# Kernel tuning notes

Measured on AMD Instinct MI355X. Metric: run time of the kernel, lower is better.

The kernel has to match this reference:

```python
import jax, jax.numpy as jnp
import numpy as np

B, S, D = 2, 2048, 2048
H, DK, DV, L = 16, 128, 128, 64


def setup_inputs() -> dict:
    key = jax.random.key(0)
    ks = jax.random.split(key, 16)
    sc = lambda fan_in: 1.0 / np.sqrt(fan_in)
    inp = {
        "queries": jax.random.normal(ks[0], (B, S, D), jnp.float32),
        "keys": jax.random.normal(ks[1], (B, S, D), jnp.float32),
        "values": jax.random.normal(ks[2], (B, S, D), jnp.float32),
        # weights stored [in, out]
        "Wq": jax.random.normal(ks[3], (D, DK * H), jnp.float32) * sc(D),
        "bq": jnp.zeros((DK * H,), jnp.float32),
        "Wlk": jax.random.normal(ks[4], (D, L * H), jnp.float32) * sc(D),
        "blk": jnp.zeros((L * H,), jnp.float32),
        "Wlv": jax.random.normal(ks[5], (D, L * H), jnp.float32) * sc(D),
        "blv": jnp.zeros((L * H,), jnp.float32),
        "Wkr": jax.random.normal(ks[6], (L, DK), jnp.float32) * sc(L),
        "bkr": jnp.zeros((DK,), jnp.float32),
        "Wvr": jax.random.normal(ks[7], (L, DV), jnp.float32) * sc(L),
        "bvr": jnp.zeros((DV,), jnp.float32),
        "Wo": jax.random.normal(ks[8], (DV * H, D), jnp.float32) * sc(DV * H),
        "bo": jnp.zeros((D,), jnp.float32),
    }
    return inp


def reference(queries, keys, values, Wq, bq, Wlk, blk, Wlv, blv, Wkr, bkr, Wvr, bvr, Wo, bo):
    b, sq, _ = queries.shape
    sk = keys.shape[1]
    # query projection -> [b, h, sq, dk]
    q = (queries @ Wq + bq).reshape(b, sq, H, DK).transpose(0, 2, 1, 3)
    # low-rank latent KV -> [b, sk, h, L]
    lat_k = (keys @ Wlk + blk).reshape(b, sk, H, L)
    lat_v = (values @ Wlv + blv).reshape(b, sk, H, L)
    # reconstruction -> [b, h, sk, dk/dv]
    k = (lat_k @ Wkr + bkr).transpose(0, 2, 1, 3)
    v = (lat_v @ Wvr + bvr).transpose(0, 2, 1, 3)
    scores = jnp.einsum("bhqd,bhkd->bhqk", q, k) / np.sqrt(DK).astype(np.float32)
    causal = jnp.triu(jnp.ones((sq, sk), dtype=bool), k=1)
    scores = jnp.where(causal, -jnp.inf, scores)
    attn = jax.nn.softmax(scores, axis=-1)
    out = jnp.einsum("bhqk,bhkd->bhqd", attn, v)
    out = out.transpose(0, 2, 1, 3).reshape(b, sq, H * DV)
    return out @ Wo + bo
```

## Files before the change

kernel.cpp:

```cpp
#include <hip/hip_runtime.h>
#include <hip/hip_bf16.h>

#define B_SZ    2
#define S_LEN   2048
#define D_MODEL 2048
#define N_HEADS 16
#define D_HEAD  128
#define L_RANK  64
#define M_ROWS  (B_SZ * S_LEN)
#define KD      2048
#define NT      (KD / 32)
#define NTK     (KD / 64)

typedef short          bf16x8 __attribute__((ext_vector_type(8)));
typedef float          f32x4  __attribute__((ext_vector_type(4)));
typedef float          f32x16 __attribute__((ext_vector_type(16)));
typedef unsigned short us4v   __attribute__((ext_vector_type(4)));
typedef unsigned short us8v   __attribute__((ext_vector_type(8)));
typedef unsigned int   u32x4  __attribute__((ext_vector_type(4)));

#define SCALE_Q 0.127517432f

static __device__ __forceinline__ unsigned short f2bf(float f) {
    unsigned int u = __float_as_uint(f);
    u += 0x7FFFu + ((u >> 16) & 1u);
    return (unsigned short)(u >> 16);
}

static __device__ __forceinline__ void gload16(const void* g, void* l) {
    __builtin_amdgcn_global_load_lds(
        (const __attribute__((address_space(1))) unsigned int*)g,
        (__attribute__((address_space(3))) unsigned int*)l, 16, 0, 0);
}

static __device__ __forceinline__ bf16x8 ds_read128(const unsigned short* p) {
    bf16x8 r;
    unsigned int a = (unsigned int)(size_t)
        (const __attribute__((address_space(3))) unsigned short*)p;
    asm volatile("ds_read_b128 %0, %1" : "=&v"(r) : "v"(a));
    return r;
}

static __device__ __forceinline__ float exp2_hw(float x) {
    float r; asm("v_exp_f32 %0, %1" : "=v"(r) : "v"(x)); return r;
}
static __device__ __forceinline__ unsigned int cvtpk_bf16(float a, float b) {
    unsigned int r; asm("v_cvt_pk_bf16_f32 %0, %1, %2" : "=v"(r) : "v"(a), "v"(b)); return r;
}

__global__ __launch_bounds__(256) void prep_kernel(
    const float* __restrict__ q_in, const float* __restrict__ k_in,
    const float* __restrict__ v_in,
    const float* __restrict__ Wq, const float* __restrict__ Wlk,
    const float* __restrict__ Wlv, const float* __restrict__ Wo,
    const float* __restrict__ Wkr, const float* __restrict__ Wvr,
    unsigned short* __restrict__ q_o, unsigned short* __restrict__ k_o,
    unsigned short* __restrict__ v_o,
    unsigned short* __restrict__ WqT, unsigned short* __restrict__ WlkT,
    unsigned short* __restrict__ WlvT, unsigned short* __restrict__ WoT,
    unsigned short* __restrict__ WkrT, unsigned short* __restrict__ WvrT)
{
    __shared__ float tl[64][69];
    const int bid = blockIdx.x, tid = threadIdx.x;

    if (bid < 12288) {
        const int z = bid >> 12;
        const float* in = z == 0 ? q_in : (z == 1 ? k_in : v_in);
        unsigned short* out = z == 0 ? q_o : (z == 1 ? k_o : v_o);
        size_t i = ((size_t)(bid & 4095) * 256 + tid) * 8;
        float4 a = *(const float4*)&in[i];
        float4 b = *(const float4*)&in[i + 4];
        us8v o = { f2bf(a.x), f2bf(a.y), f2bf(a.z), f2bf(a.w),
                   f2bf(b.x), f2bf(b.y), f2bf(b.z), f2bf(b.w) };
        *(us8v*)&out[i] = o;
    } else if (bid < 16384) {
        const int t = bid - 12288;
        const int z = t >> 10;
        const int y = (t & 1023) >> 5, x = t & 31;
        const int Nz = (z == 1 || z == 2) ? 1024 : 2048;
        if (x * 64 >= Nz) return;
        const float* W = z == 0 ? Wq : (z == 1 ? Wlk : (z == 2 ? Wlv : Wo));
        unsigned short* WT = z == 0 ? WqT : (z == 1 ? WlkT : (z == 2 ? WlvT : WoT));
        const int k0 = y * 64, n0 = x * 64;
        #pragma unroll
        for (int c = 0; c < 4; ++c) {
            int idx = c * 256 + tid;
            int r = idx >> 4, c4 = (idx & 15) * 4;
            float4 v = *(const float4*)&W[(size_t)(k0 + r) * Nz + n0 + c4];
            tl[r][c4] = v.x; tl[r][c4 + 1] = v.y; tl[r][c4 + 2] = v.z; tl[r][c4 + 3] = v.w;
        }
        __syncthreads();
        #pragma unroll
        for (int c = 0; c < 2; ++c) {
            int idx = c * 256 + tid;
            int nr = idx >> 3, s = idx & 7;
            us8v o;
            #pragma unroll
            for (int j = 0; j < 8; ++j) o[j] = f2bf(tl[s * 8 + j][nr]);
            *(us8v*)&WT[(size_t)(n0 + nr) * KD + k0 + s * 8] = o;
        }
    } else {
        #pragma unroll 1
        for (int t2 = 0; t2 < 2; ++t2) {
            const float* W = t2 ? Wvr : Wkr;
            unsigned short* WT = t2 ? WvrT : WkrT;
            for (int i = 0; i < 32; ++i) {
                int e = i * 256 + tid;
                int d = e >> 6, l = e & 63;
                WT[d * 64 + l] = f2bf(W[l * 128 + d]);
            }
        }
    }
}

__global__ __launch_bounds__(512) void stage1_8p_kernel(
    const unsigned short* __restrict__ Aq, const unsigned short* __restrict__ Ak,
    const unsigned short* __restrict__ Av,
    const unsigned short* __restrict__ WqT, const unsigned short* __restrict__ WlkT,
    const unsigned short* __restrict__ WlvT,
    const float* __restrict__ bq, const float* __restrict__ blk,
    const float* __restrict__ blv,
    unsigned short* __restrict__ q_bf, unsigned short* __restrict__ lat_k,
    unsigned short* __restrict__ lat_v)
{
    __shared__ unsigned short Al[2][2][256 * 32];
    __shared__ unsigned short Bl[2][2][256 * 32];

    const int bid = blockIdx.x;
    const int swz = (bid & 7) * 32 + (bid >> 3);
    int z, rem, row0, col0, Nz;
    if (swz < 128)      { z = 0; rem = swz;       row0 = (rem >> 3) * 256; col0 = (rem & 7) * 256; Nz = 2048; }
    else if (swz < 192) { z = 1; rem = swz - 128; row0 = (rem >> 2) * 256; col0 = (rem & 3) * 256; Nz = 1024; }
    else                { z = 2; rem = swz - 192; row0 = (rem >> 2) * 256; col0 = (rem & 3) * 256; Nz = 1024; }

    const unsigned short* A    = z == 0 ? Aq  : (z == 1 ? Ak   : Av);
    const unsigned short* Bt   = z == 0 ? WqT : (z == 1 ? WlkT : WlvT);
    const float*          bias = z == 0 ? bq  : (z == 1 ? blk  : blv);
    unsigned short*       C    = z == 0 ? q_bf : (z == 1 ? lat_k : lat_v);

    const int tid = threadIdx.x;
    const int lane = tid & 63, wid = tid >> 6;
    const int lr = lane & 15, lg = lane >> 4;
    const int wm = wid >> 2, wn = wid & 3;

    const int lin0 = tid, lin1 = 512 + tid;
    const int rS0 = lin0 >> 2, rS1 = lin1 >> 2;
    const int cS0 = (lin0 & 3) ^ ((rS0 >> 1) & 3);
    const int cS1 = (lin1 & 3) ^ ((rS1 >> 1) & 3);
    const unsigned short* aS0 = A  + (size_t)(row0 + rS0) * KD + cS0 * 8;
    const unsigned short* aS1 = A  + (size_t)(row0 + rS1) * KD + cS1 * 8;
    const unsigned short* bS0 = Bt + (size_t)(col0 + rS0) * KD + cS0 * 8;
    const unsigned short* bS1 = Bt + (size_t)(col0 + rS1) * KD + cS1 * 8;
    const int d0 = lin0 * 8, d1 = lin1 * 8;

    int aoff[8], boff[4];
    #pragma unroll
    for (int m = 0; m < 8; ++m) {
        int row = wm * 128 + m * 16 + lr;
        aoff[m] = row * 32 + ((lg ^ ((row >> 1) & 3)) * 8);
    }
    #pragma unroll
    for (int n = 0; n < 4; ++n) {
        int row = wn * 64 + n * 16 + lr;
        boff[n] = row * 32 + ((lg ^ ((row >> 1) & 3)) * 8);
    }

    f32x4 acc[8][4];
    #pragma unroll
    for (int m = 0; m < 8; ++m)
        #pragma unroll
        for (int n = 0; n < 4; ++n) acc[m][n] = (f32x4){0.f, 0.f, 0.f, 0.f};

#define STAGE_A(buf, kh, kt) do { \
        gload16(aS0 + (size_t)(kt) * 64 + (kh) * 32, &Al[buf][kh][d0]); \
        gload16(aS1 + (size_t)(kt) * 64 + (kh) * 32, &Al[buf][kh][d1]); } while (0)
#define STAGE_B(buf, kh, kt) do { \
        gload16(bS0 + (size_t)(kt) * 64 + (kh) * 32, &Bl[buf][kh][d0]); \
        gload16(bS1 + (size_t)(kt) * 64 + (kh) * 32, &Bl[buf][kh][d1]); } while (0)

    STAGE_A(0, 0, 0); STAGE_B(0, 0, 0); STAGE_A(0, 1, 0); STAGE_B(0, 1, 0);

    #pragma unroll 1
    for (int t = 0; t < NTK; ++t) {
        const int cur = t & 1, nxt = cur ^ 1;
        const bool more = (t + 1 < NTK);

        asm volatile("s_waitcnt vmcnt(4)" ::: "memory");
        __builtin_amdgcn_s_barrier();
        asm volatile("" ::: "memory");

        bf16x8 af[8], bf0, bf1;
        if (more) STAGE_A(nxt, 0, t + 1);
        #pragma unroll
        for (int m = 0; m < 8; ++m) af[m] = ds_read128(&Al[cur][0][aoff[m]]);
        bf0 = ds_read128(&Bl[cur][0][boff[0]]);
        bf1 = ds_read128(&Bl[cur][0][boff[1]]);
        asm volatile("s_waitcnt lgkmcnt(0)" ::: "memory");
        __builtin_amdgcn_sched_barrier(0);
        __builtin_amdgcn_s_setprio(1);
        #pragma unroll
        for (int m = 0; m < 8; ++m) {
            acc[m][0] = __builtin_amdgcn_mfma_f32_16x16x32_bf16(af[m], bf0, acc[m][0], 0, 0, 0);
            acc[m][1] = __builtin_amdgcn_mfma_f32_16x16x32_bf16(af[m], bf1, acc[m][1], 0, 0, 0);
        }
        __builtin_amdgcn_s_setprio(0);

        if (more) STAGE_B(nxt, 0, t + 1);
        bf0 = ds_read128(&Bl[cur][0][boff[2]]);
        bf1 = ds_read128(&Bl[cur][0][boff[3]]);
        asm volatile("s_waitcnt lgkmcnt(0)" ::: "memory");
        __builtin_amdgcn_sched_barrier(0);
        __builtin_amdgcn_s_setprio(1);
        #pragma unroll
        for (int m = 0; m < 8; ++m) {
            acc[m][2] = __builtin_amdgcn_mfma_f32_16x16x32_bf16(af[m], bf0, acc[m][2], 0, 0, 0);
            acc[m][3] = __builtin_amdgcn_mfma_f32_16x16x32_bf16(af[m], bf1, acc[m][3], 0, 0, 0);
        }
        __builtin_amdgcn_s_setprio(0);

        if (more) asm volatile("s_waitcnt vmcnt(4)" ::: "memory");
        else      asm volatile("s_waitcnt vmcnt(0)" ::: "memory");
        __builtin_amdgcn_s_barrier();
        asm volatile("" ::: "memory");

        if (more) STAGE_A(nxt, 1, t + 1);
        #pragma unroll
        for (int m = 0; m < 8; ++m) af[m] = ds_read128(&Al[cur][1][aoff[m]]);
        bf0 = ds_read128(&Bl[cur][1][boff[0]]);
        bf1 = ds_read128(&Bl[cur][1][boff[1]]);
        asm volatile("s_waitcnt lgkmcnt(0)" ::: "memory");
        __builtin_amdgcn_sched_barrier(0);
        __builtin_amdgcn_s_setprio(1);
        #pragma unroll
        for (int m = 0; m < 8; ++m) {
            acc[m][0] = __builtin_amdgcn_mfma_f32_16x16x32_bf16(af[m], bf0, acc[m][0], 0, 0, 0);
            acc[m][1] = __builtin_amdgcn_mfma_f32_16x16x32_bf16(af[m], bf1, acc[m][1], 0, 0, 0);
        }
        __builtin_amdgcn_s_setprio(0);

        if (more) STAGE_B(nxt, 1, t + 1);
        bf0 = ds_read128(&Bl[cur][1][boff[2]]);
        bf1 = ds_read128(&Bl[cur][1][boff[3]]);
        asm volatile("s_waitcnt lgkmcnt(0)" ::: "memory");
        __builtin_amdgcn_sched_barrier(0);
        __builtin_amdgcn_s_setprio(1);
        #pragma unroll
        for (int m = 0; m < 8; ++m) {
            acc[m][2] = __builtin_amdgcn_mfma_f32_16x16x32_bf16(af[m], bf0, acc[m][2], 0, 0, 0);
            acc[m][3] = __builtin_amdgcn_mfma_f32_16x16x32_bf16(af[m], bf1, acc[m][3], 0, 0, 0);
        }
        __builtin_amdgcn_s_setprio(0);
    }
#undef STAGE_A
#undef STAGE_B

    float bv[4];
    #pragma unroll
    for (int n = 0; n < 4; ++n) bv[n] = bias[col0 + wn * 64 + n * 16 + lr];
    const float omul = (z == 0) ? SCALE_Q : 1.0f;

    #pragma unroll
    for (int m = 0; m < 8; ++m) {
        #pragma unroll
        for (int n = 0; n < 4; ++n) {
            const int col = col0 + wn * 64 + n * 16 + lr;
            const int rowb = row0 + wm * 128 + m * 16 + lg * 4;
            #pragma unroll
            for (int j = 0; j < 4; ++j)
                C[(size_t)(rowb + j) * Nz + col] = f2bf((acc[m][n][j] + bv[n]) * omul);
        }
    }
}

__global__ __launch_bounds__(256) void recon_kernel(
    const unsigned short* __restrict__ lat_k, const unsigned short* __restrict__ lat_v,
    const unsigned short* __restrict__ WkrT, const unsigned short* __restrict__ WvrT,
    const float* __restrict__ bkr, const float* __restrict__ bvr,
    unsigned short* __restrict__ k_bf, unsigned short* __restrict__ v_t)
{
    __shared__ unsigned short Alds[128 * 64];
    __shared__ unsigned short Blds[128 * 64];

    const int flat = blockIdx.x;
    const int swz = (flat & 7) * 128 + (flat >> 3);
    const int z = swz >> 9;
    const int rem = swz & 511;
    const int h = rem >> 5;
    const int r0 = (rem & 31) * 128;

    const unsigned short* lat = z ? lat_v : lat_k;
    const unsigned short* WT  = z ? WvrT : WkrT;
    const float* bias = z ? bvr : bkr;

    const int tid = threadIdx.x;
    const int lane = tid & 63, wid = tid >> 6;
    const int lr = lane & 15, lg = lane >> 4;
    const int wm = wid >> 1, wn = wid & 1;

    #pragma unroll
    for (int c = 0; c < 4; ++c) {
        int e = c * 256 + tid;
        int row = e >> 3, pc = e & 7;
        gload16(lat + (size_t)(r0 + row) * 1024 + h * 64 + ((pc ^ (row & 7)) * 8),
                Alds + e * 8);
    }
    #pragma unroll
    for (int c = 0; c < 4; ++c) {
        int e = c * 256 + tid;
        int d = e >> 3, pc = e & 7;
        gload16(WT + (size_t)d * 64 + ((pc ^ (d & 7)) * 8), Blds + e * 8);
    }
    __syncthreads();

    f32x4 acc[4][4];
    #pragma unroll
    for (int m = 0; m < 4; ++m)
        #pragma unroll
        for (int n = 0; n < 4; ++n) acc[m][n] = (f32x4){0.f, 0.f, 0.f, 0.f};

    #pragma unroll
    for (int ks = 0; ks < 2; ++ks) {
        bf16x8 af[4], bfv[4];
        #pragma unroll
        for (int m = 0; m < 4; ++m) {
            int row = wm * 64 + m * 16 + lr;
            af[m] = *(const bf16x8*)&Alds[row * 64 + (((ks * 4 + lg) ^ (row & 7)) * 8)];
        }
        #pragma unroll
        for (int n = 0; n < 4; ++n) {
            int row = wn * 64 + n * 16 + lr;
            bfv[n] = *(const bf16x8*)&Blds[row * 64 + (((ks * 4 + lg) ^ (row & 7)) * 8)];
        }
        #pragma unroll
        for (int m = 0; m < 4; ++m)
            #pragma unroll
            for (int n = 0; n < 4; ++n)
                acc[m][n] = __builtin_amdgcn_mfma_f32_16x16x32_bf16(af[m], bfv[n], acc[m][n], 0, 0, 0);
    }

    const int b = r0 >> 11;
    float bv[4];
    #pragma unroll
    for (int n = 0; n < 4; ++n) bv[n] = bias[wn * 64 + n * 16 + lr];

    #pragma unroll
    for (int m = 0; m < 4; ++m) {
        #pragma unroll
        for (int n = 0; n < 4; ++n) {
            const int d = wn * 64 + n * 16 + lr;
            const int rowb = r0 + wm * 64 + m * 16 + lg * 4;
            if (z == 0) {
                #pragma unroll
                for (int j = 0; j < 4; ++j)
                    k_bf[(size_t)(rowb + j) * D_MODEL + h * D_HEAD + d] =
                        f2bf(acc[m][n][j] + bv[n]);
            } else {
                us4v o = { f2bf(acc[m][n][0] + bv[n]), f2bf(acc[m][n][1] + bv[n]),
                           f2bf(acc[m][n][2] + bv[n]), f2bf(acc[m][n][3] + bv[n]) };
                *(us4v*)&v_t[((size_t)(b * 16 + h) * 128 + d) * 2048 + (rowb & 2047)] = o;
            }
        }
    }
}

__global__ __launch_bounds__(256) void out_gemm_kernel(
    const unsigned short* __restrict__ A,
    const unsigned short* __restrict__ Bt,
    const float* __restrict__ bias,
    float* __restrict__ C)
{
    __shared__ unsigned short Al[2][128 * 32];
    __shared__ unsigned short Bl[2][128 * 32];

    const int flat = blockIdx.x;
    const int swz = (flat & 7) * 64 + (flat >> 3);
    const int row0 = (swz >> 4) * 128, col0 = (swz & 15) * 128;

    const int tid = threadIdx.x;
    const int lane = tid & 63, wid = tid >> 6;
    const int lr = lane & 15, lg = lane >> 4;
    const int wr = wid >> 1, wc = wid & 1;

    const unsigned short* ag[2];
    const unsigned short* bg[2];
    unsigned short* alp[2][2];
    unsigned short* blp[2][2];
    #pragma unroll
    for (int c = 0; c < 2; ++c) {
        int idx = wid * 128 + c * 64 + lane;
        int row = idx >> 2, p = idx & 3;
        int sp = p ^ ((row >> 1) & 3);
        ag[c] = A  + (size_t)(row0 + row) * KD + sp * 8;
        bg[c] = Bt + (size_t)(col0 + row) * KD + sp * 8;
        alp[0][c] = Al[0] + idx * 8;  alp[1][c] = Al[1] + idx * 8;
        blp[0][c] = Bl[0] + idx * 8;  blp[1][c] = Bl[1] + idx * 8;
    }
    const int sx = (lr >> 1) & 3;
    const int abase = (wr * 64 + lr) * 32 + ((lg ^ sx) * 8);
    const int bbase = (wc * 64 + lr) * 32 + ((lg ^ sx) * 8);

    f32x4 acc[4][4];
    #pragma unroll
    for (int m = 0; m < 4; ++m)
        #pragma unroll
        for (int n = 0; n < 4; ++n) acc[m][n] = (f32x4){0.f, 0.f, 0.f, 0.f};

    #pragma unroll
    for (int c = 0; c < 2; ++c) { gload16(ag[c], alp[0][c]); gload16(bg[c], blp[0][c]); }
    __syncthreads();

    #pragma unroll 1
    for (int t = 0; t < NT; ++t) {
        const int cur = t & 1, nxt = cur ^ 1;
        if (t + 1 < NT) {
            #pragma unroll
            for (int c = 0; c < 2; ++c) {
                gload16(ag[c] + (size_t)(t + 1) * 32, alp[nxt][c]);
                gload16(bg[c] + (size_t)(t + 1) * 32, blp[nxt][c]);
            }
        }
        bf16x8 af[4], bfv[4];
        #pragma unroll
        for (int m = 0; m < 4; ++m) af[m]  = *(const bf16x8*)&Al[cur][abase + m * 512];
        #pragma unroll
        for (int n = 0; n < 4; ++n) bfv[n] = *(const bf16x8*)&Bl[cur][bbase + n * 512];
        __builtin_amdgcn_s_setprio(1);
        #pragma unroll
        for (int m = 0; m < 4; ++m)
            #pragma unroll
            for (int n = 0; n < 4; ++n)
                acc[m][n] = __builtin_amdgcn_mfma_f32_16x16x32_bf16(af[m], bfv[n], acc[m][n], 0, 0, 0);
        __builtin_amdgcn_s_setprio(0);
        __syncthreads();
    }

    float bv[4];
    #pragma unroll
    for (int n = 0; n < 4; ++n) bv[n] = bias[col0 + wc * 64 + n * 16 + lr];
    #pragma unroll
    for (int m = 0; m < 4; ++m)
        #pragma unroll
        for (int n = 0; n < 4; ++n) {
            const int col = col0 + wc * 64 + n * 16 + lr;
            const int rowb = row0 + wr * 64 + m * 16 + lg * 4;
            #pragma unroll
            for (int j = 0; j < 4; ++j)
                C[(size_t)(rowb + j) * D_MODEL + col] = acc[m][n][j] + bv[n];
        }
}

static __device__ __forceinline__ void flash_stage(
    const unsigned short* __restrict__ kgh,
    const unsigned short* __restrict__ vtb,
    unsigned short* Kl, unsigned short* Vl, int kv0, int tid)
{
    #pragma unroll
    for (int c = 0; c < 4; ++c) {
        int idx = c * 256 + tid;
        int r = idx >> 4, ch = idx & 15;
        gload16(kgh + (size_t)(kv0 + r) * D_MODEL + ((ch ^ (r & 7)) * 8), Kl + idx * 8);
    }
    #pragma unroll
    for (int c = 0; c < 4; ++c) {
        int idx = c * 256 + tid;
        int d = idx >> 3, ch = idx & 7;
        gload16(vtb + (size_t)d * S_LEN + kv0 + ((ch ^ (d & 7)) * 8), Vl + idx * 8);
    }
}

__global__ __launch_bounds__(256, 2) void flash_kernel(
    const unsigned short* __restrict__ Q,
    const unsigned short* __restrict__ Kg,
    const unsigned short* __restrict__ Vt,
    unsigned short* __restrict__ Og)
{
    __shared__ unsigned short Klds[2][64 * 128];
    __shared__ unsigned short Vlds[2][128 * 64];

    const int tid = threadIdx.x;
    const int lane = tid & 63, wid = tid >> 6;
    const int lc = lane & 31, hi = lane >> 5;

    const int blk = blockIdx.x;
    const int jj = blk >> 5;
    const int qt = (jj < 8) ? (15 - jj) : (jj - 8);
    const int bh = blk & 31;
    const int b = bh >> 4, h = bh & 15;
    const size_t base = (size_t)b * S_LEN * D_MODEL;
    const unsigned short* kgh = Kg + base + h * D_HEAD;
    const unsigned short* vtb = Vt + (size_t)bh * D_HEAD * S_LEN;

    const int q0w = qt * 128 + wid * 32;
    const int qcol = q0w + lc;

    bf16x8 qf[8];
    #pragma unroll
    for (int dc = 0; dc < 8; ++dc)
        qf[dc] = *(const bf16x8*)&Q[base + (size_t)qcol * D_MODEL + h * D_HEAD + dc * 16 + hi * 8];

    f32x16 o_acc[4];
    #pragma unroll
    for (int dt = 0; dt < 4; ++dt)
        #pragma unroll
        for (int r = 0; r < 16; ++r) o_acc[dt][r] = 0.f;
    float m_r = -3e38f, l_r = 0.f;

    const int kxor = lc & 7;
    const int nt = 2 * qt + 2;

    flash_stage(kgh, vtb, Klds[0], Vlds[0], 0, tid);

    #pragma unroll 1
    for (int t = 0; t < nt; ++t) {
        const int bb = t & 1;
        const int kv0 = t * 64;
        __syncthreads();
        if (t + 1 < nt)
            flash_stage(kgh, vtb, Klds[bb ^ 1], Vlds[bb ^ 1], (t + 1) * 64, tid);

        f32x16 s0a, s0b, s1a, s1b;
        #pragma unroll
        for (int r = 0; r < 16; ++r) { s0a[r] = 0.f; s0b[r] = 0.f; s1a[r] = 0.f; s1b[r] = 0.f; }
        __builtin_amdgcn_s_setprio(1);
        #pragma unroll
        for (int dc = 0; dc < 4; ++dc) {
            bf16x8 kf0 = *(const bf16x8*)&Klds[bb][lc * 128 + (((dc * 2 + hi) ^ kxor) * 8)];
            bf16x8 kf1 = *(const bf16x8*)&Klds[bb][(32 + lc) * 128 + (((dc * 2 + hi) ^ kxor) * 8)];
            s0a = __builtin_amdgcn_mfma_f32_32x32x16_bf16(kf0, qf[dc], s0a, 0, 0, 0);
            s1a = __builtin_amdgcn_mfma_f32_32x32x16_bf16(kf1, qf[dc], s1a, 0, 0, 0);
        }
        #pragma unroll
        for (int dc = 4; dc < 8; ++dc) {
            bf16x8 kf0 = *(const bf16x8*)&Klds[bb][lc * 128 + (((dc * 2 + hi) ^ kxor) * 8)];
            bf16x8 kf1 = *(const bf16x8*)&Klds[bb][(32 + lc) * 128 + (((dc * 2 + hi) ^ kxor) * 8)];
            s0b = __builtin_amdgcn_mfma_f32_32x32x16_bf16(kf0, qf[dc], s0b, 0, 0, 0);
            s1b = __builtin_amdgcn_mfma_f32_32x32x16_bf16(kf1, qf[dc], s1b, 0, 0, 0);
        }
        __builtin_amdgcn_s_setprio(0);
        f32x16 s0 = s0a + s0b;
        f32x16 s1 = s1a + s1b;

        if (t >= nt - 2) {
            #pragma unroll
            for (int r = 0; r < 16; ++r) {
                int krow = (r & 3) + 8 * (r >> 2) + 4 * hi;
                if (kv0 + krow > qcol)      s0[r] = -3e38f;
                if (kv0 + 32 + krow > qcol) s1[r] = -3e38f;
            }
        }

        float mt[8];
        #pragma unroll
        for (int i = 0; i < 8; ++i)
            mt[i] = fmaxf(fmaxf(s0[2 * i], s0[2 * i + 1]), fmaxf(s1[2 * i], s1[2 * i + 1]));
        float mA = fmaxf(fmaxf(mt[0], mt[1]), fmaxf(mt[2], mt[3]));
        float mB = fmaxf(fmaxf(mt[4], mt[5]), fmaxf(mt[6], mt[7]));
        float sm = fmaxf(mA, mB);
        sm = fmaxf(sm, __shfl_xor(sm, 32));

        if (__any(sm > m_r + 11.5f)) {
            float mnew = fmaxf(m_r, sm);
            float alpha = exp2_hw(m_r - mnew);
            l_r *= alpha;
            m_r = mnew;
            #pragma unroll
            for (int r = 0; r < 16; ++r) {
                float av = __shfl(alpha, (r & 3) + 8 * (r >> 2) + 4 * hi);
                #pragma unroll
                for (int dt = 0; dt < 4; ++dt) o_acc[dt][r] *= av;
            }
        }

        #pragma unroll
        for (int r = 0; r < 16; ++r) {
            s0[r] = exp2_hw(s0[r] - m_r);
            s1[r] = exp2_hw(s1[r] - m_r);
        }
        float st[8];
        #pragma unroll
        for (int i = 0; i < 8; ++i)
            st[i] = (s0[2 * i] + s0[2 * i + 1]) + (s1[2 * i] + s1[2 * i + 1]);
        l_r += ((st[0] + st[1]) + (st[2] + st[3])) + ((st[4] + st[5]) + (st[6] + st[7]));

        #pragma unroll
        for (int t32 = 0; t32 < 2; ++t32) {
            const f32x16& s = t32 ? s1 : s0;
            unsigned int c0[4], c1[4];
            #pragma unroll
            for (int g = 0; g < 4; ++g) {
                c0[g] = cvtpk_bf16(s[4 * g],     s[4 * g + 1]);
                c1[g] = cvtpk_bf16(s[4 * g + 2], s[4 * g + 3]);
            }
            #pragma unroll
            for (int kt = 0; kt < 2; ++kt) {
                unsigned int sel0 = hi ? c0[2 * kt] : c0[2 * kt + 1];
                unsigned int sel1 = hi ? c1[2 * kt] : c1[2 * kt + 1];
                unsigned int o0 = (unsigned int)__shfl_xor((int)sel0, 32);
                unsigned int o1 = (unsigned int)__shfl_xor((int)sel1, 32);
                u32x4 uu;
                uu.x = hi ? o0 : c0[2 * kt];
                uu.y = hi ? o1 : c1[2 * kt];
                uu.z = hi ? c0[2 * kt + 1] : o0;
                uu.w = hi ? c1[2 * kt + 1] : o1;
                bf16x8 pf = __builtin_bit_cast(bf16x8, uu);
                __builtin_amdgcn_s_setprio(1);
                #pragma unroll
                for (int dt = 0; dt < 4; ++dt) {
                    bf16x8 vf = *(const bf16x8*)
                        &Vlds[bb][(dt * 32 + lc) * 64 + (((t32 * 4 + kt * 2 + hi) ^ kxor) * 8)];
                    o_acc[dt] = __builtin_amdgcn_mfma_f32_32x32x16_bf16(pf, vf, o_acc[dt], 0, 0, 0);
                }
                __builtin_amdgcn_s_setprio(0);
            }
        }
    }

    float lt = l_r + __shfl_xor(l_r, 32);
    float inv = 1.0f / lt;
    #pragma unroll
    for (int r = 0; r < 16; ++r) {
        int qrow = (r & 3) + 8 * (r >> 2) + 4 * hi;
        float iv = __shfl(inv, qrow);
        #pragma unroll
        for (int dt = 0; dt < 4; ++dt)
            Og[base + (size_t)(q0w + qrow) * D_MODEL + h * D_HEAD + dt * 32 + lc] =
                f2bf(o_acc[dt][r] * iv);
    }
}

extern "C" void kernel_launch(void* const* d_in, const int* in_sizes, int n_in,
                              void* d_out, int out_size, void* d_ws, size_t ws_size,
                              hipStream_t stream)
{
    const float* queries = (const float*)d_in[0];
    const float* keys    = (const float*)d_in[1];
    const float* values  = (const float*)d_in[2];
    const float* Wq  = (const float*)d_in[3];
    const float* bq  = (const float*)d_in[4];
    const float* Wlk = (const float*)d_in[5];
    const float* blk = (const float*)d_in[6];
    const float* Wlv = (const float*)d_in[7];
    const float* blv = (const float*)d_in[8];
    const float* Wkr = (const float*)d_in[9];
    const float* bkr = (const float*)d_in[10];
    const float* Wvr = (const float*)d_in[11];
    const float* bvr = (const float*)d_in[12];
    const float* Wo  = (const float*)d_in[13];
    const float* bo  = (const float*)d_in[14];
    float* out = (float*)d_out;

    char* ws = (char*)d_ws;
    const size_t MB = 1024 * 1024;
    unsigned short* abf_q = (unsigned short*)(ws);
    unsigned short* abf_k = (unsigned short*)(ws + 16 * MB);
    unsigned short* abf_v = (unsigned short*)(ws + 32 * MB);
    unsigned short* q_bf  = (unsigned short*)(ws + 48 * MB);
    unsigned short* k_bf  = (unsigned short*)(ws + 64 * MB);
    unsigned short* v_t   = (unsigned short*)(ws + 80 * MB);
    unsigned short* lat_k = (unsigned short*)(ws + 96 * MB);
    unsigned short* lat_v = (unsigned short*)(ws + 104 * MB);
    unsigned short* WqT   = (unsigned short*)(ws + 112 * MB);
    unsigned short* WlkT  = (unsigned short*)(ws + 120 * MB);
    unsigned short* WlvT  = (unsigned short*)(ws + 124 * MB);
    unsigned short* WkrT  = (unsigned short*)(ws + 128 * MB);
    unsigned short* WvrT  = WkrT + 128 * 64;
    unsigned short* WoT   = (unsigned short*)(ws + 129 * MB);
    unsigned short* ao    = abf_q;

    prep_kernel<<<16385, 256, 0, stream>>>(
        queries, keys, values, Wq, Wlk, Wlv, Wo, Wkr, Wvr,
        abf_q, abf_k, abf_v, WqT, WlkT, WlvT, WoT, WkrT, WvrT);

    stage1_8p_kernel<<<256, 512, 0, stream>>>(
        abf_q, abf_k, abf_v, WqT, WlkT, WlvT, bq, blk, blv,
        q_bf, lat_k, lat_v);

    recon_kernel<<<1024, 256, 0, stream>>>(
        lat_k, lat_v, WkrT, WvrT, bkr, bvr, k_bf, v_t);

    flash_kernel<<<512, 256, 0, stream>>>(q_bf, k_bf, v_t, ao);

    out_gemm_kernel<<<512, 256, 0, stream>>>(ao, WoT, bo, out);
}
```

Measured before the change: 242.2 us.

## Replace output GEMM with 8-wave 128x256 tile and phased load/MFMA pipeline

The output projection GEMM moves from 128x128 tiles on 4 waves to 128x256 tiles on 8 waves, with 64-wide K steps split into two 32-wide halves. Global-to-LDS loads for the next step are interleaved between MFMA phases using explicit vmcnt/lgkmcnt waits and raw barriers, the same scheme the stage1 8-phase kernel uses. The goal is more reuse per tile, fewer grid blocks, and better overlap of memory traffic with matrix math. In exchange it uses more LDS per block and relies on hand-tuned waitcnt counts that must match the number of loads in flight.

```diff
diff --git a/kernel.cpp b/kernel.cpp
--- a/kernel.cpp
+++ b/kernel.cpp
@@ -272,6 +272,151 @@
     }
 }
 
+__global__ __launch_bounds__(512) void out_gemm8p_kernel(
+    const unsigned short* __restrict__ A,
+    const unsigned short* __restrict__ Bt,
+    const float* __restrict__ bias,
+    float* __restrict__ C)
+{
+    __shared__ unsigned short Al[2][2][128 * 32];
+    __shared__ unsigned short Bl[2][2][256 * 32];
+
+    const int bid = blockIdx.x;
+    const int swz = (bid & 7) * 32 + (bid >> 3);
+    const int row0 = (swz >> 3) * 128, col0 = (swz & 7) * 256;
+
+    const int tid = threadIdx.x;
+    const int lane = tid & 63, wid = tid >> 6;
+    const int lr = lane & 15, lg = lane >> 4;
+    const int wm = wid >> 2, wn = wid & 3;
+
+    const int rA = tid >> 2;
+    const int cA = (tid & 3) ^ ((rA >> 1) & 3);
+    const unsigned short* aS = A + (size_t)(row0 + rA) * KD + cA * 8;
+    const int dA = tid * 8;
+    const int lin0 = tid, lin1 = 512 + tid;
+    const int rB0 = lin0 >> 2, rB1 = lin1 >> 2;
+    const int cB0 = (lin0 & 3) ^ ((rB0 >> 1) & 3);
+    const int cB1 = (lin1 & 3) ^ ((rB1 >> 1) & 3);
+    const unsigned short* bS0 = Bt + (size_t)(col0 + rB0) * KD + cB0 * 8;
+    const unsigned short* bS1 = Bt + (size_t)(col0 + rB1) * KD + cB1 * 8;
+    const int dB0 = lin0 * 8, dB1 = lin1 * 8;
+
+    int aoff[4], boff[4];
+    #pragma unroll
+    for (int m = 0; m < 4; ++m) {
+        int row = wm * 64 + m * 16 + lr;
+        aoff[m] = row * 32 + ((lg ^ ((row >> 1) & 3)) * 8);
+    }
+    #pragma unroll
+    for (int n = 0; n < 4; ++n) {
+        int row = wn * 64 + n * 16 + lr;
+        boff[n] = row * 32 + ((lg ^ ((row >> 1) & 3)) * 8);
+    }
+
+    f32x4 acc[4][4];
+    #pragma unroll
+    for (int m = 0; m < 4; ++m)
+        #pragma unroll
+        for (int n = 0; n < 4; ++n) acc[m][n] = (f32x4){0.f, 0.f, 0.f, 0.f};
+
+#define STAGE_A(buf, kh, kt) \
+        gload16(aS + (size_t)(kt) * 64 + (kh) * 32, &Al[buf][kh][dA])
+#define STAGE_B(buf, kh, kt) do { \
+        gload16(bS0 + (size_t)(kt) * 64 + (kh) * 32, &Bl[buf][kh][dB0]); \
+        gload16(bS1 + (size_t)(kt) * 64 + (kh) * 32, &Bl[buf][kh][dB1]); } while (0)
+
+    STAGE_A(0, 0, 0); STAGE_B(0, 0, 0); STAGE_A(0, 1, 0); STAGE_B(0, 1, 0);
+
+    #pragma unroll 1
+    for (int t = 0; t < NTK; ++t) {
+        const int cur = t & 1, nxt = cur ^ 1;
+        const bool more = (t + 1 < NTK);
+
+        asm volatile("s_waitcnt vmcnt(3)" ::: "memory");
+        __builtin_amdgcn_s_barrier();
+        asm volatile("" ::: "memory");
+
+        bf16x8 af[4], bf0, bf1;
+        if (more) STAGE_A(nxt, 0, t + 1);
+        #pragma unroll
+        for (int m = 0; m < 4; ++m) af[m] = ds_read128(&Al[cur][0][aoff[m]]);
+        bf0 = ds_read128(&Bl[cur][0][boff[0]]);
+        bf1 = ds_read128(&Bl[cur][0][boff[1]]);
+        asm volatile("s_waitcnt lgkmcnt(0)" ::: "memory");
+        __builtin_amdgcn_sched_barrier(0);
+        __builtin_amdgcn_s_setprio(1);
+        #pragma unroll
+        for (int m = 0; m < 4; ++m) {
+            acc[m][0] = __builtin_amdgcn_mfma_f32_16x16x32_bf16(af[m], bf0, acc[m][0], 0, 0, 0);
+            acc[m][1] = __builtin_amdgcn_mfma_f32_16x16x32_bf16(af[m], bf1, acc[m][1], 0, 0, 0);
+        }
+        __builtin_amdgcn_s_setprio(0);
+
+        if (more) STAGE_B(nxt, 0, t + 1);
+        bf0 = ds_read128(&Bl[cur][0][boff[2]]);
+        bf1 = ds_read128(&Bl[cur][0][boff[3]]);
+        asm volatile("s_waitcnt lgkmcnt(0)" ::: "memory");
+        __builtin_amdgcn_sched_barrier(0);
+        __builtin_amdgcn_s_setprio(1);
+        #pragma unroll
+        for (int m = 0; m < 4; ++m) {
+            acc[m][2] = __builtin_amdgcn_mfma_f32_16x16x32_bf16(af[m], bf0, acc[m][2], 0, 0, 0);
+            acc[m][3] = __builtin_amdgcn_mfma_f32_16x16x32_bf16(af[m], bf1, acc[m][3], 0, 0, 0);
+        }
+        __builtin_amdgcn_s_setprio(0);
+
+        if (more) asm volatile("s_waitcnt vmcnt(3)" ::: "memory");
+        else      asm volatile("s_waitcnt vmcnt(0)" ::: "memory");
+        __builtin_amdgcn_s_barrier();
+        asm volatile("" ::: "memory");
+
+        if (more) STAGE_A(nxt, 1, t + 1);
+        #pragma unroll
+        for (int m = 0; m < 4; ++m) af[m] = ds_read128(&Al[cur][1][aoff[m]]);
+        bf0 = ds_read128(&Bl[cur][1][boff[0]]);
+        bf1 = ds_read128(&Bl[cur][1][boff[1]]);
+        asm volatile("s_waitcnt lgkmcnt(0)" ::: "memory");
+        __builtin_amdgcn_sched_barrier(0);
+        __builtin_amdgcn_s_setprio(1);
+        #pragma unroll
+        for (int m = 0; m < 4; ++m) {
+            acc[m][0] = __builtin_amdgcn_mfma_f32_16x16x32_bf16(af[m], bf0, acc[m][0], 0, 0, 0);
+            acc[m][1] = __builtin_amdgcn_mfma_f32_16x16x32_bf16(af[m], bf1, acc[m][1], 0, 0, 0);
+        }
+        __builtin_amdgcn_s_setprio(0);
+
+        if (more) STAGE_B(nxt, 1, t + 1);
+        bf0 = ds_read128(&Bl[cur][1][boff[2]]);
+        bf1 = ds_read128(&Bl[cur][1][boff[3]]);
+        asm volatile("s_waitcnt lgkmcnt(0)" ::: "memory");
+        __builtin_amdgcn_sched_barrier(0);
+        __builtin_amdgcn_s_setprio(1);
+        #pragma unroll
+        for (int m = 0; m < 4; ++m) {
+            acc[m][2] = __builtin_amdgcn_mfma_f32_16x16x32_bf16(af[m], bf0, acc[m][2], 0, 0, 0);
+            acc[m][3] = __builtin_amdgcn_mfma_f32_16x16x32_bf16(af[m], bf1, acc[m][3], 0, 0, 0);
+        }
+        __builtin_amdgcn_s_setprio(0);
+    }
+#undef STAGE_A
+#undef STAGE_B
+
+    float bv[4];
+    #pragma unroll
+    for (int n = 0; n < 4; ++n) bv[n] = bias[col0 + wn * 64 + n * 16 + lr];
+    #pragma unroll
+    for (int m = 0; m < 4; ++m)
+        #pragma unroll
+        for (int n = 0; n < 4; ++n) {
+            const int col = col0 + wn * 64 + n * 16 + lr;
+            const int rowb = row0 + wm * 64 + m * 16 + lg * 4;
+            #pragma unroll
+            for (int j = 0; j < 4; ++j)
+                C[(size_t)(rowb + j) * D_MODEL + col] = acc[m][n][j] + bv[n];
+        }
+}
+
 __global__ __launch_bounds__(256) void recon_kernel(
     const unsigned short* __restrict__ lat_k, const unsigned short* __restrict__ lat_v,
     const unsigned short* __restrict__ WkrT, const unsigned short* __restrict__ WvrT,
@@ -361,92 +506,6 @@
             }
         }
     }
-}
-
-__global__ __launch_bounds__(256) void out_gemm_kernel(
-    const unsigned short* __restrict__ A,
-    const unsigned short* __restrict__ Bt,
-    const float* __restrict__ bias,
-    float* __restrict__ C)
-{
-    __shared__ unsigned short Al[2][128 * 32];
-    __shared__ unsigned short Bl[2][128 * 32];
-
-    const int flat = blockIdx.x;
-    const int swz = (flat & 7) * 64 + (flat >> 3);
-    const int row0 = (swz >> 4) * 128, col0 = (swz & 15) * 128;
-
-    const int tid = threadIdx.x;
-    const int lane = tid & 63, wid = tid >> 6;
-    const int lr = lane & 15, lg = lane >> 4;
-    const int wr = wid >> 1, wc = wid & 1;
-
-    const unsigned short* ag[2];
-    const unsigned short* bg[2];
-    unsigned short* alp[2][2];
-    unsigned short* blp[2][2];
-    #pragma unroll
-    for (int c = 0; c < 2; ++c) {
-        int idx = wid * 128 + c * 64 + lane;
-        int row = idx >> 2, p = idx & 3;
-        int sp = p ^ ((row >> 1) & 3);
-        ag[c] = A  + (size_t)(row0 + row) * KD + sp * 8;
-        bg[c] = Bt + (size_t)(col0 + row) * KD + sp * 8;
-        alp[0][c] = Al[0] + idx * 8;  alp[1][c] = Al[1] + idx * 8;
-        blp[0][c] = Bl[0] + idx * 8;  blp[1][c] = Bl[1] + idx * 8;
-    }
-    const int sx = (lr >> 1) & 3;
-    const int abase = (wr * 64 + lr) * 32 + ((lg ^ sx) * 8);
-    const int bbase = (wc * 64 + lr) * 32 + ((lg ^ sx) * 8);
-
-    f32x4 acc[4][4];
-    #pragma unroll
-    for (int m = 0; m < 4; ++m)
-        #pragma unroll
-        for (int n = 0; n < 4; ++n) acc[m][n] = (f32x4){0.f, 0.f, 0.f, 0.f};
-
-    #pragma unroll
-    for (int c = 0; c < 2; ++c) { gload16(ag[c], alp[0][c]); gload16(bg[c], blp[0][c]); }
-    __syncthreads();
-
-    #pragma unroll 1
-    for (int t = 0; t < NT; ++t) {
-        const int cur = t & 1, nxt = cur ^ 1;
-        if (t + 1 < NT) {
-            #pragma unroll
-            for (int c = 0; c < 2; ++c) {
-                gload16(ag[c] + (size_t)(t + 1) * 32, alp[nxt][c]);
-                gload16(bg[c] + (size_t)(t + 1) * 32, blp[nxt][c]);
-            }
-        }
-        bf16x8 af[4], bfv[4];
-        #pragma unroll
-        for (int m = 0; m < 4; ++m) af[m]  = *(const bf16x8*)&Al[cur][abase + m * 512];
-        #pragma unroll
-        for (int n = 0; n < 4; ++n) bfv[n] = *(const bf16x8*)&Bl[cur][bbase + n * 512];
-        __builtin_amdgcn_s_setprio(1);
-        #pragma unroll
-        for (int m = 0; m < 4; ++m)
-            #pragma unroll
-            for (int n = 0; n < 4; ++n)
-                acc[m][n] = __builtin_amdgcn_mfma_f32_16x16x32_bf16(af[m], bfv[n], acc[m][n], 0, 0, 0);
-        __builtin_amdgcn_s_setprio(0);
-        __syncthreads();
-    }
-
-    float bv[4];
-    #pragma unroll
-    for (int n = 0; n < 4; ++n) bv[n] = bias[col0 + wc * 64 + n * 16 + lr];
-    #pragma unroll
-    for (int m = 0; m < 4; ++m)
-        #pragma unroll
-        for (int n = 0; n < 4; ++n) {
-            const int col = col0 + wc * 64 + n * 16 + lr;
-            const int rowb = row0 + wr * 64 + m * 16 + lg * 4;
-            #pragma unroll
-            for (int j = 0; j < 4; ++j)
-                C[(size_t)(rowb + j) * D_MODEL + col] = acc[m][n][j] + bv[n];
-        }
 }
 
 static __device__ __forceinline__ void flash_stage(
@@ -680,5 +739,5 @@
 
     flash_kernel<<<512, 256, 0, stream>>>(q_bf, k_bf, v_t, ao);
 
-    out_gemm_kernel<<<512, 256, 0, stream>>>(ao, WoT, bo, out);
-}
+    out_gemm8p_kernel<<<256, 512, 0, stream>>>(ao, WoT, bo, out);
+}
```

New measurement: 234.0 us. 1.04x faster.
